# Kernel optimization log

Hardware: AMD Instinct MI355X
Metric: run time of the kernel (lower is better)

The kernel has to match this reference:

```python
import jax, jax.numpy as jnp
import numpy as np

DIM, H, C = 1024, 16, 64  # dim, num_heads, head_width
B, N = 2, 2048
EPS = 1e-5


def setup_inputs() -> dict:
    key = jax.random.key(0)
    ks = jax.random.split(key, 8)
    x = jax.random.normal(ks[0], (B, N, DIM), dtype=jnp.float32)
    bias = jax.random.normal(ks[1], (B, H, N, N), dtype=jnp.float32)
    mask = jax.random.randint(ks[2], (B, N), 0, 2, dtype=jnp.int32)
    s = DIM ** -0.5
    return {
        'x': x,
        'bias': bias,
        'mask': mask,
        'ln_w': jnp.ones((DIM,), jnp.float32),
        'ln_b': jnp.zeros((DIM,), jnp.float32),
        'w_qkv': jax.random.normal(ks[3], (3 * DIM, DIM), jnp.float32) * s,
        'w_o': jax.random.normal(ks[4], (DIM, DIM), jnp.float32) * s,
        'b_o': jnp.zeros((DIM,), jnp.float32),
        'w_g': jax.random.normal(ks[5], (DIM, DIM), jnp.float32) * s,
        'b_g': jnp.ones((DIM,), jnp.float32),
    }


def reference(x, bias, mask, ln_w, ln_b, w_qkv, w_o, b_o, w_g, b_g):
    # LayerNorm (eps=1e-5)
    mu = jnp.mean(x, axis=-1, keepdims=True)
    var = jnp.mean(jnp.square(x - mu), axis=-1, keepdims=True)
    xn = (x - mu) * jax.lax.rsqrt(var + EPS) * ln_w + ln_b

    # QKV projection (no bias): (B,N,3*DIM) -> (B,H,N,3C), chunk last dim
    t = jnp.einsum('bnd,ed->bne', xn, w_qkv)
    t = t.reshape(B, N, H, 3 * C).transpose(0, 2, 1, 3)  # (B,H,N,3C)
    q, k, v = t[..., :C], t[..., C:2 * C], t[..., 2 * C:]
    q = q * (C ** -0.5)

    # Biased, masked attention scores
    a = jnp.einsum('bhqc,bhkc->bhqk', q, k) + bias
    a = jnp.where(mask[:, None, None, :] == 0, -jnp.inf, a)
    a = jax.nn.softmax(a, axis=-1)

    y = jnp.einsum('bhqk,bhkc->bqhc', a, v).reshape(B, N, DIM)

    # Sigmoid gate from normalized x, then output projection
    g = jax.nn.sigmoid(jnp.einsum('bnd,ed->bne', xn, w_g) + b_g)
    y = g * y
    return jnp.einsum('bnd,ed->bne', y, w_o) + b_o
```

## Files before the change

### kernel.cpp

```cpp
#include <hip/hip_runtime.h>

#define DIMD 1024
#define NHEAD 16
#define CHD 64
#define BBATCH 2
#define NSEQ 2048
#define NTOK 4096
#define KDIM 1024

typedef __attribute__((ext_vector_type(4))) float f32x4;
typedef __attribute__((ext_vector_type(8))) short bf16x8;

__device__ __forceinline__ unsigned short f2bf(float f){
  unsigned int u = __float_as_uint(f);
  u += 0x7fffu + ((u >> 16) & 1u);
  return (unsigned short)(u >> 16);
}
__device__ __forceinline__ float bf2f(unsigned short u){
  return __uint_as_float(((unsigned int)u) << 16);
}

__device__ __forceinline__ void gl2lds16(const void* g, void* l){
  __builtin_amdgcn_global_load_lds(
      (const __attribute__((address_space(1))) unsigned int*)g,
      (__attribute__((address_space(3))) unsigned int*)l, 16, 0, 0);
}

__global__ __launch_bounds__(256) void ln_kernel(const float* __restrict__ x,
    const float* __restrict__ lw, const float* __restrict__ lb,
    unsigned short* __restrict__ xn){
  int row = blockIdx.x;
  int t = threadIdx.x;
  const float4* xr = (const float4*)(x + (size_t)row * DIMD);
  float4 v = xr[t];
  float s  = v.x + v.y + v.z + v.w;
  float s2 = v.x*v.x + v.y*v.y + v.z*v.z + v.w*v.w;
#pragma unroll
  for (int m = 1; m < 64; m <<= 1){
    s  += __shfl_xor(s,  m, 64);
    s2 += __shfl_xor(s2, m, 64);
  }
  __shared__ float red[8];
  int wv = t >> 6;
  if ((t & 63) == 0){ red[wv] = s; red[wv + 4] = s2; }
  __syncthreads();
  s  = red[0] + red[1] + red[2] + red[3];
  s2 = red[4] + red[5] + red[6] + red[7];
  float mu  = s  * (1.0f / DIMD);
  float var = s2 * (1.0f / DIMD) - mu * mu;
  float rs  = rsqrtf(var + 1e-5f);
  float4 w  = ((const float4*)lw)[t];
  float4 bb = ((const float4*)lb)[t];
  ushort4 o;
  o.x = f2bf((v.x - mu) * rs * w.x + bb.x);
  o.y = f2bf((v.y - mu) * rs * w.y + bb.y);
  o.z = f2bf((v.z - mu) * rs * w.z + bb.z);
  o.w = f2bf((v.w - mu) * rs * w.w + bb.w);
  ((ushort4*)xn)[(size_t)row * 256 + t] = o;
}

__global__ __launch_bounds__(256) void convert_w(const float* __restrict__ wqkv,
    const float* __restrict__ wg, const float* __restrict__ wo,
    unsigned short* __restrict__ Wpack, unsigned short* __restrict__ Wo){
  int i = blockIdx.x * 256 + threadIdx.x;
  const int NQP   = 4096 * 1024 / 4;
  const int NQQKV = 3072 * 1024 / 4;
  float4 v; unsigned short* dst;
  if (i < NQP){
    const float* src = (i < NQQKV) ? (wqkv + (size_t)i * 4)
                                   : (wg + (size_t)(i - NQQKV) * 4);
    v = *(const float4*)src;
    dst = Wpack + (size_t)i * 4;
  } else {
    int j = i - NQP;
    v = ((const float4*)wo)[j];
    dst = Wo + (size_t)j * 4;
  }
  ushort4 o = { f2bf(v.x), f2bf(v.y), f2bf(v.z), f2bf(v.w) };
  *(ushort4*)dst = o;
}

__device__ __forceinline__ void gemm_stage(const unsigned short* __restrict__ A,
    const unsigned short* __restrict__ Bm, int m0, int n0, int kb, char* lds, int tid){
#pragma unroll
  for (int i = 0; i < 4; i++){
    int c  = i * 256 + tid;
    int cc = c & 511;
    int r  = cc >> 2, k4 = cc & 3;
    const unsigned short* src =
        ((c >> 9) ? (Bm + (size_t)(n0 + r) * KDIM) : (A + (size_t)(m0 + r) * KDIM))
        + kb + k4 * 8;
    gl2lds16(src, lds + c * 16);
  }
}

__device__ __forceinline__ void gemm_main(const unsigned short* __restrict__ A,
    const unsigned short* __restrict__ Bm, int m0, int n0, char* lds,
    f32x4 acc[4][4], int wm, int wn, int l16, int quad){
  int tid = threadIdx.x;
  gemm_stage(A, Bm, m0, n0, 0, lds, tid);
  for (int kt = 0; kt < 32; kt++){
    __syncthreads();
    if (kt + 1 < 32)
      gemm_stage(A, Bm, m0, n0, (kt + 1) * 32, lds + ((kt + 1) & 1) * 16384, tid);
    const char* Ab = lds + (kt & 1) * 16384;
    const char* Bb = Ab + 8192;
    bf16x8 af[4], bfr[4];
#pragma unroll
    for (int t2 = 0; t2 < 4; t2++){
      af[t2]  = *(const bf16x8*)(Ab + (wm + t2 * 16 + l16) * 64 + quad * 16);
      bfr[t2] = *(const bf16x8*)(Bb + (wn + t2 * 16 + l16) * 64 + quad * 16);
    }
#pragma unroll
    for (int mt = 0; mt < 4; mt++)
#pragma unroll
      for (int nt = 0; nt < 4; nt++)
        acc[mt][nt] = __builtin_amdgcn_mfma_f32_16x16x32_bf16(af[mt], bfr[nt], acc[mt][nt], 0, 0, 0);
  }
}

__global__ __launch_bounds__(256) void gemm_qkvg(const unsigned short* __restrict__ xn,
    const unsigned short* __restrict__ Wpack, const float* __restrict__ bg,
    unsigned short* __restrict__ Q, unsigned short* __restrict__ Ko,
    unsigned short* __restrict__ Vt, unsigned short* __restrict__ g){
  __shared__ char lds[32768];
  int tid = threadIdx.x, lane = tid & 63, wave = tid >> 6;
  int l16 = lane & 15, quad = lane >> 4;
  int wm = (wave & 1) * 64, wn = (wave >> 1) * 64;
  int m0 = blockIdx.y * 128, n0 = blockIdx.x * 128;
  f32x4 acc[4][4];
#pragma unroll
  for (int i = 0; i < 4; i++)
#pragma unroll
    for (int j = 0; j < 4; j++) acc[i][j] = (f32x4){0.f, 0.f, 0.f, 0.f};
  gemm_main(xn, Wpack, m0, n0, lds, acc, wm, wn, l16, quad);
#pragma unroll
  for (int mt = 0; mt < 4; mt++){
#pragma unroll
    for (int nt = 0; nt < 4; nt++){
      int col = n0 + wn + nt * 16 + l16;
#pragma unroll
      for (int reg = 0; reg < 4; reg++){
        int row = m0 + wm + mt * 16 + quad * 4 + reg;
        float val = acc[mt][nt][reg];
        int b = row >> 11, n = row & 2047;
        if (col < 3072){
          int h = col / 192;
          int r = col - h * 192;
          int bh = b * 16 + h;
          if (r < 64)
            Q[((size_t)bh * 2048 + n) * 64 + r] = f2bf(val * 0.125f);
          else if (r < 128)
            Ko[((size_t)bh * 2048 + n) * 64 + (r - 64)] = f2bf(val);
          else
            Vt[((size_t)bh * 64 + (r - 128)) * 2048 + n] = f2bf(val);
        } else {
          int d = col - 3072;
          float gv = 1.0f / (1.0f + __expf(-(val + bg[d])));
          g[(size_t)row * 1024 + d] = f2bf(gv);
        }
      }
    }
  }
}

__device__ __forceinline__ void attn_stage(const unsigned short* __restrict__ Kbh,
    const unsigned short* __restrict__ Vtbh, int kb, char* Kdst, char* Vdst, int tid){
#pragma unroll
  for (int i = 0; i < 2; i++){
    int l = i * 256 + tid;
    int n = l >> 3, cc = (l & 7) ^ (n & 7);
    gl2lds16(Kbh + (size_t)(kb + n) * 64 + cc * 8, Kdst + l * 16);
  }
#pragma unroll
  for (int i = 0; i < 2; i++){
    int l = i * 256 + tid;
    int c = l >> 3, cc = (l & 7) ^ (c & 7);
    gl2lds16(Vtbh + (size_t)c * 2048 + kb + cc * 8, Vdst + l * 16);
  }
}

__global__ __launch_bounds__(256) void attn_kernel(
    const unsigned short* __restrict__ Q, const unsigned short* __restrict__ Ko,
    const unsigned short* __restrict__ Vt, const float* __restrict__ bias,
    const int* __restrict__ mask, const unsigned short* __restrict__ g,
    unsigned short* __restrict__ yg){
  __shared__ char smem[40960];
  int tid = threadIdx.x, lane = tid & 63, wave = tid >> 6;
  int l16 = lane & 15, quad = lane >> 4;
  int qt = blockIdx.x, bh = blockIdx.y;
  int b = bh >> 4, h = bh & 15;

  const unsigned short* Qbh  = Q  + (size_t)bh * 2048 * 64;
  const unsigned short* Kbh  = Ko + (size_t)bh * 2048 * 64;
  const unsigned short* Vtbh = Vt + (size_t)bh * 64 * 2048;
  const float* biasw = bias + (size_t)bh * 2048 * 2048 + (size_t)(qt * 64 + wave * 16) * 2048;
  const int* maskb = mask + b * 2048;
  char* Pw = smem + 32768 + wave * 2048;

  bf16x8 qf[2];
  {
    const unsigned short* qrow = Qbh + (size_t)(qt * 64 + wave * 16 + l16) * 64;
    qf[0] = *(const bf16x8*)(qrow + quad * 8);
    qf[1] = *(const bf16x8*)(qrow + 32 + quad * 8);
  }

  f32x4 yacc[4];
#pragma unroll
  for (int ct = 0; ct < 4; ct++) yacc[ct] = (f32x4){0.f, 0.f, 0.f, 0.f};
  float m_run[4] = {-1e30f, -1e30f, -1e30f, -1e30f};
  float l_run[4] = {0.f, 0.f, 0.f, 0.f};

  attn_stage(Kbh, Vtbh, 0, smem, smem + 16384, tid);

  for (int kt = 0; kt < 32; kt++){
    __syncthreads();
    int kb = kt * 64;
    float brow[4][4]; int mk[4];
#pragma unroll
    for (int nt = 0; nt < 4; nt++){
      mk[nt] = maskb[kb + nt * 16 + l16];
#pragma unroll
      for (int reg = 0; reg < 4; reg++)
        brow[nt][reg] = biasw[(size_t)(quad * 4 + reg) * 2048 + kb + nt * 16 + l16];
    }
    if (kt + 1 < 32)
      attn_stage(Kbh, Vtbh, kb + 64, smem + ((kt + 1) & 1) * 8192,
                 smem + 16384 + ((kt + 1) & 1) * 8192, tid);
    const char* Kb_ = smem + (kt & 1) * 8192;
    const char* Vb_ = smem + 16384 + (kt & 1) * 8192;

    f32x4 s[4];
#pragma unroll
    for (int nt = 0; nt < 4; nt++) s[nt] = (f32x4){0.f, 0.f, 0.f, 0.f};
#pragma unroll
    for (int kk = 0; kk < 2; kk++)
#pragma unroll
      for (int nt = 0; nt < 4; nt++){
        int n = nt * 16 + l16;
        bf16x8 kf = *(const bf16x8*)(Kb_ + n * 128 + ((((kk << 2) + quad) ^ (n & 7)) << 4));
        s[nt] = __builtin_amdgcn_mfma_f32_16x16x32_bf16(qf[kk], kf, s[nt], 0, 0, 0);
      }
#pragma unroll
    for (int nt = 0; nt < 4; nt++){
      bool ok = (mk[nt] != 0);
#pragma unroll
      for (int reg = 0; reg < 4; reg++){
        float v = s[nt][reg] + brow[nt][reg];
        s[nt][reg] = ok ? v : -1e30f;
      }
    }
    float mt_[4];
#pragma unroll
    for (int reg = 0; reg < 4; reg++)
      mt_[reg] = fmaxf(fmaxf(s[0][reg], s[1][reg]), fmaxf(s[2][reg], s[3][reg]));
#pragma unroll
    for (int reg = 0; reg < 4; reg++)
#pragma unroll
      for (int off = 1; off < 16; off <<= 1)
        mt_[reg] = fmaxf(mt_[reg], __shfl_xor(mt_[reg], off, 64));
    float alpha[4], psum[4];
#pragma unroll
    for (int reg = 0; reg < 4; reg++){
      float mn = fmaxf(m_run[reg], mt_[reg]);
      alpha[reg] = __expf(m_run[reg] - mn);
      m_run[reg] = mn;
      psum[reg] = 0.f;
    }
#pragma unroll
    for (int nt = 0; nt < 4; nt++){
      int n = nt * 16 + l16;
#pragma unroll
      for (int reg = 0; reg < 4; reg++){
        float p = __expf(s[nt][reg] - m_run[reg]);
        psum[reg] += p;
        int r = quad * 4 + reg;
        *(unsigned short*)(Pw + r * 128 + (((n >> 3) ^ (r & 7)) << 4) + ((n & 7) << 1)) = f2bf(p);
      }
    }
#pragma unroll
    for (int reg = 0; reg < 4; reg++){
#pragma unroll
      for (int off = 1; off < 16; off <<= 1)
        psum[reg] += __shfl_xor(psum[reg], off, 64);
      l_run[reg] = l_run[reg] * alpha[reg] + psum[reg];
    }
#pragma unroll
    for (int ct = 0; ct < 4; ct++)
#pragma unroll
      for (int reg = 0; reg < 4; reg++)
        yacc[ct][reg] *= alpha[reg];
    asm volatile("s_waitcnt lgkmcnt(0)" ::: "memory");
#pragma unroll
    for (int kk = 0; kk < 2; kk++){
      bf16x8 pf = *(const bf16x8*)(Pw + l16 * 128 + ((((kk << 2) + quad) ^ (l16 & 7)) << 4));
#pragma unroll
      for (int ct = 0; ct < 4; ct++){
        int c = ct * 16 + l16;
        bf16x8 vf = *(const bf16x8*)(Vb_ + c * 128 + ((((kk << 2) + quad) ^ (c & 7)) << 4));
        yacc[ct] = __builtin_amdgcn_mfma_f32_16x16x32_bf16(pf, vf, yacc[ct], 0, 0, 0);
      }
    }
  }
  float inv[4];
#pragma unroll
  for (int reg = 0; reg < 4; reg++) inv[reg] = 1.0f / l_run[reg];
#pragma unroll
  for (int ct = 0; ct < 4; ct++){
    int d = h * 64 + ct * 16 + l16;
#pragma unroll
    for (int reg = 0; reg < 4; reg++){
      int token = b * 2048 + qt * 64 + wave * 16 + quad * 4 + reg;
      float gv = bf2f(g[(size_t)token * 1024 + d]);
      yg[(size_t)token * 1024 + d] = f2bf(yacc[ct][reg] * inv[reg] * gv);
    }
  }
}

__global__ __launch_bounds__(256) void gemm_out(const unsigned short* __restrict__ yg,
    const unsigned short* __restrict__ Wo, const float* __restrict__ bo,
    float* __restrict__ out){
  __shared__ char lds[32768];
  int tid = threadIdx.x, lane = tid & 63, wave = tid >> 6;
  int l16 = lane & 15, quad = lane >> 4;
  int wm = (wave & 1) * 64, wn = (wave >> 1) * 64;
  int m0 = blockIdx.y * 128, n0 = blockIdx.x * 128;
  f32x4 acc[4][4];
#pragma unroll
  for (int i = 0; i < 4; i++)
#pragma unroll
    for (int j = 0; j < 4; j++) acc[i][j] = (f32x4){0.f, 0.f, 0.f, 0.f};
  gemm_main(yg, Wo, m0, n0, lds, acc, wm, wn, l16, quad);
#pragma unroll
  for (int mt = 0; mt < 4; mt++){
#pragma unroll
    for (int nt = 0; nt < 4; nt++){
      int col = n0 + wn + nt * 16 + l16;
#pragma unroll
      for (int reg = 0; reg < 4; reg++){
        int row = m0 + wm + mt * 16 + quad * 4 + reg;
        out[(size_t)row * 1024 + col] = acc[mt][nt][reg] + bo[col];
      }
    }
  }
}

extern "C" void kernel_launch(void* const* d_in, const int* in_sizes, int n_in,
                              void* d_out, int out_size, void* d_ws, size_t ws_size,
                              hipStream_t stream){
  const float* x    = (const float*)d_in[0];
  const float* bias = (const float*)d_in[1];
  const int*   mask = (const int*)d_in[2];
  const float* lnw  = (const float*)d_in[3];
  const float* lnb  = (const float*)d_in[4];
  const float* wqkv = (const float*)d_in[5];
  const float* wo   = (const float*)d_in[6];
  const float* bo   = (const float*)d_in[7];
  const float* wg   = (const float*)d_in[8];
  const float* bg   = (const float*)d_in[9];
  float* out = (float*)d_out;

  char* ws = (char*)d_ws;
  unsigned short* xn    = (unsigned short*)(ws);
  unsigned short* Wpack = (unsigned short*)(ws + (8u  << 20));
  unsigned short* Wob   = (unsigned short*)(ws + (16u << 20));
  unsigned short* Qb    = (unsigned short*)(ws + (18u << 20));
  unsigned short* Kb    = (unsigned short*)(ws + (26u << 20));
  unsigned short* Vtb   = (unsigned short*)(ws + (34u << 20));
  unsigned short* gb    = (unsigned short*)(ws + (42u << 20));
  unsigned short* ygb   = (unsigned short*)(ws + (50u << 20));

  ln_kernel<<<dim3(4096), dim3(256), 0, stream>>>(x, lnw, lnb, xn);
  convert_w<<<dim3(5120), dim3(256), 0, stream>>>(wqkv, wg, wo, Wpack, Wob);
  gemm_qkvg<<<dim3(32, 32), dim3(256), 0, stream>>>(xn, Wpack, bg, Qb, Kb, Vtb, gb);
  attn_kernel<<<dim3(32, 32), dim3(256), 0, stream>>>(Qb, Kb, Vtb, bias, mask, gb, ygb);
  gemm_out<<<dim3(8, 32), dim3(256), 0, stream>>>(ygb, Wob, bo, out);
}
```

Before: 879.6 us.

## Prefetch attention bias one tile ahead, use exp2/DPP reductions, merge prep kernels

The attention loop now loads the bias and mask for the next key tile while the current one is processed, using register double-buffering and a manually unrolled two-step loop, so the large fp32 bias stream's global load latency is hidden. Softmax moves to base 2: Q is prescaled by log2(e), bias is folded in with an fma, exp2 replaces expf, and the row max/sum reductions use DPP moves instead of shuffles. P uses a cheaper rounding to bf16 and the final reciprocal uses the hardware rcp. The layernorm and weight-conversion kernels are merged into one launch. The costs are higher register pressure from the doubled bias buffers and slightly different rounding.

Measured after the change: 855.3 us. -2.8%, faster.

```diff
diff --git a/kernel.cpp b/kernel.cpp
--- a/kernel.cpp
+++ b/kernel.cpp
@@ -7,6 +7,7 @@
 #define NSEQ 2048
 #define NTOK 4096
 #define KDIM 1024
+#define LOG2E 1.4426950408889634f
 
 typedef __attribute__((ext_vector_type(4))) float f32x4;
 typedef __attribute__((ext_vector_type(8))) short bf16x8;
@@ -26,58 +27,77 @@
       (__attribute__((address_space(3))) unsigned int*)l, 16, 0, 0);
 }
 
-__global__ __launch_bounds__(256) void ln_kernel(const float* __restrict__ x,
+template<int CTRL>
+__device__ __forceinline__ float dppmv(float x){
+  return __int_as_float(__builtin_amdgcn_mov_dpp(__float_as_int(x), CTRL, 0xF, 0xF, true));
+}
+__device__ __forceinline__ float rmax16(float x){
+  x = fmaxf(x, dppmv<0xB1>(x));
+  x = fmaxf(x, dppmv<0x4E>(x));
+  x = fmaxf(x, dppmv<0x141>(x));
+  x = fmaxf(x, dppmv<0x140>(x));
+  return x;
+}
+__device__ __forceinline__ float rsum16(float x){
+  x += dppmv<0xB1>(x);
+  x += dppmv<0x4E>(x);
+  x += dppmv<0x141>(x);
+  x += dppmv<0x140>(x);
+  return x;
+}
+
+__global__ __launch_bounds__(256) void pre_kernel(const float* __restrict__ x,
     const float* __restrict__ lw, const float* __restrict__ lb,
-    unsigned short* __restrict__ xn){
-  int row = blockIdx.x;
+    const float* __restrict__ wqkv, const float* __restrict__ wg,
+    const float* __restrict__ wo, unsigned short* __restrict__ xn,
+    unsigned short* __restrict__ Wpack, unsigned short* __restrict__ Wo){
+  __shared__ float red[8];
   int t = threadIdx.x;
-  const float4* xr = (const float4*)(x + (size_t)row * DIMD);
-  float4 v = xr[t];
-  float s  = v.x + v.y + v.z + v.w;
-  float s2 = v.x*v.x + v.y*v.y + v.z*v.z + v.w*v.w;
-#pragma unroll
-  for (int m = 1; m < 64; m <<= 1){
-    s  += __shfl_xor(s,  m, 64);
-    s2 += __shfl_xor(s2, m, 64);
-  }
-  __shared__ float red[8];
-  int wv = t >> 6;
-  if ((t & 63) == 0){ red[wv] = s; red[wv + 4] = s2; }
-  __syncthreads();
-  s  = red[0] + red[1] + red[2] + red[3];
-  s2 = red[4] + red[5] + red[6] + red[7];
-  float mu  = s  * (1.0f / DIMD);
-  float var = s2 * (1.0f / DIMD) - mu * mu;
-  float rs  = rsqrtf(var + 1e-5f);
-  float4 w  = ((const float4*)lw)[t];
-  float4 bb = ((const float4*)lb)[t];
-  ushort4 o;
-  o.x = f2bf((v.x - mu) * rs * w.x + bb.x);
-  o.y = f2bf((v.y - mu) * rs * w.y + bb.y);
-  o.z = f2bf((v.z - mu) * rs * w.z + bb.z);
-  o.w = f2bf((v.w - mu) * rs * w.w + bb.w);
-  ((ushort4*)xn)[(size_t)row * 256 + t] = o;
-}
-
-__global__ __launch_bounds__(256) void convert_w(const float* __restrict__ wqkv,
-    const float* __restrict__ wg, const float* __restrict__ wo,
-    unsigned short* __restrict__ Wpack, unsigned short* __restrict__ Wo){
-  int i = blockIdx.x * 256 + threadIdx.x;
-  const int NQP   = 4096 * 1024 / 4;
-  const int NQQKV = 3072 * 1024 / 4;
-  float4 v; unsigned short* dst;
-  if (i < NQP){
-    const float* src = (i < NQQKV) ? (wqkv + (size_t)i * 4)
-                                   : (wg + (size_t)(i - NQQKV) * 4);
-    v = *(const float4*)src;
-    dst = Wpack + (size_t)i * 4;
+  if (blockIdx.x < 4096){
+    int row = blockIdx.x;
+    const float4* xr = (const float4*)(x + (size_t)row * DIMD);
+    float4 v = xr[t];
+    float s  = v.x + v.y + v.z + v.w;
+    float s2 = v.x*v.x + v.y*v.y + v.z*v.z + v.w*v.w;
+#pragma unroll
+    for (int m = 1; m < 64; m <<= 1){
+      s  += __shfl_xor(s,  m, 64);
+      s2 += __shfl_xor(s2, m, 64);
+    }
+    int wv = t >> 6;
+    if ((t & 63) == 0){ red[wv] = s; red[wv + 4] = s2; }
+    __syncthreads();
+    s  = red[0] + red[1] + red[2] + red[3];
+    s2 = red[4] + red[5] + red[6] + red[7];
+    float mu  = s  * (1.0f / DIMD);
+    float var = s2 * (1.0f / DIMD) - mu * mu;
+    float rs  = rsqrtf(var + 1e-5f);
+    float4 w  = ((const float4*)lw)[t];
+    float4 bb = ((const float4*)lb)[t];
+    ushort4 o;
+    o.x = f2bf((v.x - mu) * rs * w.x + bb.x);
+    o.y = f2bf((v.y - mu) * rs * w.y + bb.y);
+    o.z = f2bf((v.z - mu) * rs * w.z + bb.z);
+    o.w = f2bf((v.w - mu) * rs * w.w + bb.w);
+    ((ushort4*)xn)[(size_t)row * 256 + t] = o;
   } else {
-    int j = i - NQP;
-    v = ((const float4*)wo)[j];
-    dst = Wo + (size_t)j * 4;
-  }
-  ushort4 o = { f2bf(v.x), f2bf(v.y), f2bf(v.z), f2bf(v.w) };
-  *(ushort4*)dst = o;
+    int i = (blockIdx.x - 4096) * 256 + t;
+    const int NQP   = 4096 * 1024 / 4;
+    const int NQQKV = 3072 * 1024 / 4;
+    float4 v; unsigned short* dst;
+    if (i < NQP){
+      const float* src = (i < NQQKV) ? (wqkv + (size_t)i * 4)
+                                     : (wg + (size_t)(i - NQQKV) * 4);
+      v = *(const float4*)src;
+      dst = Wpack + (size_t)i * 4;
+    } else {
+      int j = i - NQP;
+      v = ((const float4*)wo)[j];
+      dst = Wo + (size_t)j * 4;
+    }
+    ushort4 o = { f2bf(v.x), f2bf(v.y), f2bf(v.z), f2bf(v.w) };
+    *(ushort4*)dst = o;
+  }
 }
 
 __device__ __forceinline__ void gemm_stage(const unsigned short* __restrict__ A,
@@ -134,6 +154,7 @@
 #pragma unroll
     for (int j = 0; j < 4; j++) acc[i][j] = (f32x4){0.f, 0.f, 0.f, 0.f};
   gemm_main(xn, Wpack, m0, n0, lds, acc, wm, wn, l16, quad);
+  const float QSCALE = 0.125f * LOG2E;
 #pragma unroll
   for (int mt = 0; mt < 4; mt++){
 #pragma unroll
@@ -149,7 +170,7 @@
           int r = col - h * 192;
           int bh = b * 16 + h;
           if (r < 64)
-            Q[((size_t)bh * 2048 + n) * 64 + r] = f2bf(val * 0.125f);
+            Q[((size_t)bh * 2048 + n) * 64 + r] = f2bf(val * QSCALE);
           else if (r < 128)
             Ko[((size_t)bh * 2048 + n) * 64 + (r - 64)] = f2bf(val);
           else
@@ -211,24 +232,34 @@
   float m_run[4] = {-1e30f, -1e30f, -1e30f, -1e30f};
   float l_run[4] = {0.f, 0.f, 0.f, 0.f};
 
+  float ba[4][4], bb[4][4];
+  int mka[4], mkb[4];
   attn_stage(Kbh, Vtbh, 0, smem, smem + 16384, tid);
-
-  for (int kt = 0; kt < 32; kt++){
+#pragma unroll
+  for (int nt = 0; nt < 4; nt++){
+    mka[nt] = maskb[nt * 16 + l16];
+#pragma unroll
+    for (int reg = 0; reg < 4; reg++)
+      ba[nt][reg] = biasw[(size_t)(quad * 4 + reg) * 2048 + nt * 16 + l16];
+  }
+
+  auto body = [&](int kt, float (&cur)[4][4], int (&mcur)[4],
+                  float (&nxt)[4][4], int (&mnxt)[4]){
     __syncthreads();
     int kb = kt * 64;
-    float brow[4][4]; int mk[4];
-#pragma unroll
-    for (int nt = 0; nt < 4; nt++){
-      mk[nt] = maskb[kb + nt * 16 + l16];
-#pragma unroll
-      for (int reg = 0; reg < 4; reg++)
-        brow[nt][reg] = biasw[(size_t)(quad * 4 + reg) * 2048 + kb + nt * 16 + l16];
-    }
-    if (kt + 1 < 32)
-      attn_stage(Kbh, Vtbh, kb + 64, smem + ((kt + 1) & 1) * 8192,
-                 smem + 16384 + ((kt + 1) & 1) * 8192, tid);
-    const char* Kb_ = smem + (kt & 1) * 8192;
-    const char* Vb_ = smem + 16384 + (kt & 1) * 8192;
+    if (kt + 1 < 32){
+      attn_stage(Kbh, Vtbh, kb + 64, smem + (((kt + 1) & 1) << 13),
+                 smem + 16384 + (((kt + 1) & 1) << 13), tid);
+#pragma unroll
+      for (int nt = 0; nt < 4; nt++){
+        mnxt[nt] = maskb[kb + 64 + nt * 16 + l16];
+#pragma unroll
+        for (int reg = 0; reg < 4; reg++)
+          nxt[nt][reg] = biasw[(size_t)(quad * 4 + reg) * 2048 + kb + 64 + nt * 16 + l16];
+      }
+    }
+    const char* Kb_ = smem + ((kt & 1) << 13);
+    const char* Vb_ = smem + 16384 + ((kt & 1) << 13);
 
     f32x4 s[4];
 #pragma unroll
@@ -243,27 +274,20 @@
       }
 #pragma unroll
     for (int nt = 0; nt < 4; nt++){
-      bool ok = (mk[nt] != 0);
+      bool ok = (mcur[nt] != 0);
 #pragma unroll
       for (int reg = 0; reg < 4; reg++){
-        float v = s[nt][reg] + brow[nt][reg];
+        float v = fmaf(cur[nt][reg], LOG2E, s[nt][reg]);
         s[nt][reg] = ok ? v : -1e30f;
       }
     }
-    float mt_[4];
-#pragma unroll
-    for (int reg = 0; reg < 4; reg++)
-      mt_[reg] = fmaxf(fmaxf(s[0][reg], s[1][reg]), fmaxf(s[2][reg], s[3][reg]));
-#pragma unroll
-    for (int reg = 0; reg < 4; reg++)
-#pragma unroll
-      for (int off = 1; off < 16; off <<= 1)
-        mt_[reg] = fmaxf(mt_[reg], __shfl_xor(mt_[reg], off, 64));
     float alpha[4], psum[4];
 #pragma unroll
     for (int reg = 0; reg < 4; reg++){
-      float mn = fmaxf(m_run[reg], mt_[reg]);
-      alpha[reg] = __expf(m_run[reg] - mn);
+      float m4 = fmaxf(fmaxf(s[0][reg], s[1][reg]), fmaxf(s[2][reg], s[3][reg]));
+      m4 = rmax16(m4);
+      float mn = fmaxf(m_run[reg], m4);
+      alpha[reg] = __builtin_amdgcn_exp2f(m_run[reg] - mn);
       m_run[reg] = mn;
       psum[reg] = 0.f;
     }
@@ -272,18 +296,18 @@
       int n = nt * 16 + l16;
 #pragma unroll
       for (int reg = 0; reg < 4; reg++){
-        float p = __expf(s[nt][reg] - m_run[reg]);
+        float p = __builtin_amdgcn_exp2f(s[nt][reg] - m_run[reg]);
         psum[reg] += p;
         int r = quad * 4 + reg;
-        *(unsigned short*)(Pw + r * 128 + (((n >> 3) ^ (r & 7)) << 4) + ((n & 7) << 1)) = f2bf(p);
+        unsigned int u = __float_as_uint(p) + 0x8000u;
+        *(unsigned short*)(Pw + r * 128 + (((n >> 3) ^ (r & 7)) << 4) + ((n & 7) << 1)) =
+            (unsigned short)(u >> 16);
       }
     }
 #pragma unroll
     for (int reg = 0; reg < 4; reg++){
-#pragma unroll
-      for (int off = 1; off < 16; off <<= 1)
-        psum[reg] += __shfl_xor(psum[reg], off, 64);
-      l_run[reg] = l_run[reg] * alpha[reg] + psum[reg];
+      float ps = rsum16(psum[reg]);
+      l_run[reg] = l_run[reg] * alpha[reg] + ps;
     }
 #pragma unroll
     for (int ct = 0; ct < 4; ct++)
@@ -301,10 +325,17 @@
         yacc[ct] = __builtin_amdgcn_mfma_f32_16x16x32_bf16(pf, vf, yacc[ct], 0, 0, 0);
       }
     }
-  }
+  };
+
+#pragma unroll 1
+  for (int kt2 = 0; kt2 < 16; kt2++){
+    body(kt2 * 2,     ba, mka, bb, mkb);
+    body(kt2 * 2 + 1, bb, mkb, ba, mka);
+  }
+
   float inv[4];
 #pragma unroll
-  for (int reg = 0; reg < 4; reg++) inv[reg] = 1.0f / l_run[reg];
+  for (int reg = 0; reg < 4; reg++) inv[reg] = __builtin_amdgcn_rcpf(l_run[reg]);
 #pragma unroll
   for (int ct = 0; ct < 4; ct++){
     int d = h * 64 + ct * 16 + l16;
@@ -370,8 +401,7 @@
   unsigned short* gb    = (unsigned short*)(ws + (42u << 20));
   unsigned short* ygb   = (unsigned short*)(ws + (50u << 20));
 
-  ln_kernel<<<dim3(4096), dim3(256), 0, stream>>>(x, lnw, lnb, xn);
-  convert_w<<<dim3(5120), dim3(256), 0, stream>>>(wqkv, wg, wo, Wpack, Wob);
+  pre_kernel<<<dim3(9216), dim3(256), 0, stream>>>(x, lnw, lnb, wqkv, wg, wo, xn, Wpack, Wob);
   gemm_qkvg<<<dim3(32, 32), dim3(256), 0, stream>>>(xn, Wpack, bg, Qb, Kb, Vtb, gb);
   attn_kernel<<<dim3(32, 32), dim3(256), 0, stream>>>(Qb, Kb, Vtb, bias, mask, gb, ygb);
   gemm_out<<<dim3(8, 32), dim3(256), 0, stream>>>(ygb, Wob, bo, out);
```
